# Optimization experiments

Measured on AMD Instinct MI355X. Metric: run time of the kernel, lower is better.

## Reference

```python
import jax, jax.numpy as jnp
import numpy as np

BN_EPS = 1e-5
K = 9  # 3x3 kernel positions


def conv2d(x, w, b, pad, dil=1):
    out = jax.lax.conv_general_dilated(
        x, w, window_strides=(1, 1), padding=((pad, pad), (pad, pad)),
        rhs_dilation=(dil, dil), dimension_numbers=('NCHW', 'OIHW', 'NCHW'))
    return out + b[None, :, None, None]


def bn_relu(x, g, be, mu, var):
    inv = jax.lax.rsqrt(var + BN_EPS)
    return jax.nn.relu((x - mu[None, :, None, None]) * (g * inv)[None, :, None, None] + be[None, :, None, None])


def deform_conv(x, w_om, b_om, w, b):
    # DCNv2-style modulated deformable 3x3 conv, stride 1, pad 1, dg=1.
    B, C, H, W = x.shape
    om = conv2d(x, w_om, b_om, pad=1)               # [B, 27, H, W]
    o1, o2, m = jnp.split(om, 3, axis=1)            # dy, dx, mask logits: [B,9,H,W]
    mask = jax.nn.sigmoid(m)
    ky, kx = jnp.meshgrid(jnp.arange(3), jnp.arange(3), indexing='ij')
    ky = (ky.reshape(-1) - 1).astype(x.dtype)       # kernel offsets in {-1,0,1}
    kx = (kx.reshape(-1) - 1).astype(x.dtype)
    py = jnp.arange(H, dtype=x.dtype)[None, None, :, None] + ky[None, :, None, None] + o1  # [B,9,H,W]
    px = jnp.arange(W, dtype=x.dtype)[None, None, None, :] + kx[None, :, None, None] + o2

    y0 = jnp.floor(py); x0 = jnp.floor(px)
    wy1 = py - y0; wx1 = px - x0
    y0i = y0.astype(jnp.int32); x0i = x0.astype(jnp.int32)
    x_flat = x.reshape(B, C, H * W)

    def corner(yi, xi, wgt):
        valid = ((yi >= 0) & (yi < H) & (xi >= 0) & (xi < W)).astype(x.dtype)
        idx = jnp.clip(yi, 0, H - 1) * W + jnp.clip(xi, 0, W - 1)      # [B,9,H,W]
        g = jax.vmap(lambda xf, i: xf[:, i])(x_flat, idx.reshape(B, -1))
        g = g.reshape(B, C, K, H, W)
        return g * (wgt * valid)[:, None]

    cols = (corner(y0i,     x0i,     (1 - wy1) * (1 - wx1))
            + corner(y0i,     x0i + 1, (1 - wy1) * wx1)
            + corner(y0i + 1, x0i,     wy1 * (1 - wx1))
            + corner(y0i + 1, x0i + 1, wy1 * wx1))                       # [B,C,9,H,W]
    cols = cols * mask[:, None]
    out = jnp.einsum('bckhw,ock->bohw', cols, w.reshape(w.shape[0], C, K))
    return out + b[None, :, None, None]


def setup_inputs() -> dict:
    key = jax.random.key(0)
    ks = jax.random.split(key, 24)
    B, C, H, W = 2, 64, 256, 256
    d = {}
    d['x'] = jax.random.normal(ks[0], (B, C, H, W), jnp.float32)
    d['w_om'] = jax.random.normal(ks[1], (27, C, 3, 3), jnp.float32) * 0.01
    d['b_om'] = jax.random.normal(ks[2], (27,), jnp.float32) * 0.01
    d['w_dcn'] = jax.random.normal(ks[3], (C, C, 3, 3), jnp.float32) * 0.05
    d['b_dcn'] = jax.random.normal(ks[4], (C,), jnp.float32) * 0.05
    for i, pfx in enumerate(['bn1', 'bn2', 'bn3']):
        d[pfx + '_g'] = jax.random.uniform(ks[5 + 4 * i], (C,), jnp.float32, 0.5, 1.5)
        d[pfx + '_b'] = jax.random.normal(ks[6 + 4 * i], (C,), jnp.float32) * 0.05
        d[pfx + '_m'] = jax.random.normal(ks[7 + 4 * i], (C,), jnp.float32) * 0.05
        d[pfx + '_v'] = jax.random.uniform(ks[8 + 4 * i], (C,), jnp.float32, 0.5, 1.5)
    d['w_h'] = jax.random.normal(ks[17], (C, C, 3, 3), jnp.float32) * 0.05
    d['b_h'] = jax.random.normal(ks[18], (C,), jnp.float32) * 0.05
    d['w_w'] = jax.random.normal(ks[19], (C, C, 3, 3), jnp.float32) * 0.05
    d['b_w'] = jax.random.normal(ks[20], (C,), jnp.float32) * 0.05
    d['w3'] = jax.random.normal(ks[21], (1, C, 3, 3), jnp.float32) * 0.05
    d['b3'] = jax.random.normal(ks[22], (1,), jnp.float32) * 0.05
    return d


def reference(x, w_om, b_om, w_dcn, b_dcn,
              bn1_g, bn1_b, bn1_m, bn1_v,
              w_h, b_h, bn2_g, bn2_b, bn2_m, bn2_v,
              w_w, b_w, bn3_g, bn3_b, bn3_m, bn3_v,
              w3, b3):
    h = deform_conv(x, w_om, b_om, w_dcn, b_dcn)
    h = bn_relu(h, bn1_g, bn1_b, bn1_m, bn1_v)
    h = conv2d(h, w_h, b_h, pad=2, dil=2)
    h = bn_relu(h, bn2_g, bn2_b, bn2_m, bn2_v)
    h = conv2d(h, w_w, b_w, pad=2, dil=2)
    h = bn_relu(h, bn3_g, bn3_b, bn3_m, bn3_v)
    h = conv2d(h, w3, b3, pad=1)
    return jnp.clip(jax.nn.sigmoid(h), 1e-4, 1.0 - 1e-4)
```

## Files before the change

kernel.cpp:

```cpp
#include <hip/hip_runtime.h>
#include <math.h>

#define HH 256
#define WW 256
#define HW (HH*WW)
#define NPX (2*HW)

typedef __attribute__((ext_vector_type(8))) short bf16x8;
typedef __attribute__((ext_vector_type(8))) _Float16 f16x8;
typedef __attribute__((ext_vector_type(4))) _Float16 f16x4;
typedef __attribute__((ext_vector_type(2))) _Float16 f16x2;
typedef __attribute__((ext_vector_type(4))) float f32x4;

__device__ __forceinline__ float bf2f(short h) {
    union { unsigned u; float f; } v; v.u = ((unsigned)(unsigned short)h) << 16; return v.f;
}
__device__ __forceinline__ short f2bf(float f) {
    union { float f; unsigned u; } v; v.f = f;
    unsigned r = v.u + 0x7fffu + ((v.u >> 16) & 1u);
    return (short)(r >> 16);
}
__device__ __forceinline__ short f2hs(float f) {
    _Float16 h = (_Float16)f;
    union { _Float16 h; short s; } v; v.h = h; return v.s;
}

__global__ __launch_bounds__(256) void k_x2cl(const float* __restrict__ x,
        short* __restrict__ xcl,
        const float* __restrict__ w_om, const float* __restrict__ w_dcn,
        const float* __restrict__ w_h,  const float* __restrict__ w_w,
        const float* __restrict__ w3,
        short* __restrict__ wt_om, short* __restrict__ wt_dcn,
        short* __restrict__ wt_h,  short* __restrict__ wt_w,
        float* __restrict__ w3t) {
    __shared__ short tile[256 * 70];
    const int xx = threadIdx.x;
    const int row = blockIdx.x;
    const int b = row >> 8, y = row & 255;
#pragma unroll 8
    for (int c = 0; c < 64; ++c)
        tile[xx * 70 + c] = f2hs(x[((size_t)(b * 64 + c) << 16) + (y << 8) + xx]);
    int i = blockIdx.x * 256 + threadIdx.x;
    if (i < 64 * 576) {
        int o = i / 576, k = i - o * 576, t = k >> 6, c = k & 63;
        int kb = k >> 3, j = k & 7;
        int src = (o * 64 + c) * 9 + t;
        int dst = (kb * 64 + o) * 8 + j;
        wt_dcn[dst] = f2hs(w_dcn[src]);
        wt_h[dst]   = f2bf(w_h[src]);
        wt_w[dst]   = f2bf(w_w[src]);
        if (o < 32) wt_om[(kb * 32 + o) * 8 + j] = (o < 27) ? f2hs(w_om[src]) : (short)0;
        if (o == 0) w3t[k] = w3[c * 9 + t];
    }
    __syncthreads();
    short* op = xcl + ((row << 8) + xx) * 64;
    const int* tp = (const int*)&tile[xx * 70];
#pragma unroll
    for (int j = 0; j < 8; ++j) {
        int4 v;
        v.x = tp[j * 4 + 0]; v.y = tp[j * 4 + 1];
        v.z = tp[j * 4 + 2]; v.w = tp[j * 4 + 3];
        *(int4*)(op + j * 8) = v;
    }
}

#define XPS 72

__global__ __launch_bounds__(256) __attribute__((amdgpu_waves_per_eu(2, 4)))
void k_dcn_mfma(const short* __restrict__ xcl,
        const short* __restrict__ wom, const float* __restrict__ b_om,
        const short* __restrict__ wt,
        const float* __restrict__ bias,
        const float* __restrict__ gg, const float* __restrict__ be,
        const float* __restrict__ mu, const float* __restrict__ var,
        short* __restrict__ out_cl) {
    __shared__ short xt[256 * XPS];
    __shared__ _Float16 om_lds[64 * 32];
    const int lane = threadIdx.x & 63, wave = threadIdx.x >> 6;
    const int quad = lane >> 4, l16 = lane & 15;
    const int band = blockIdx.x & 7, idx = blockIdx.x >> 3;
    const int tr = band * 8 + (idx >> 5), tc = idx & 31;
    const int b = tr >> 5;
    const int ty0 = (tr & 31) * 8, tx0 = tc * 8;
    const int base = b << 16;
    const int hy0 = ty0 - 4, hx0 = tx0 - 4;
    {
        const int p = threadIdx.x;
        const int sy = min(max(hy0 + (p >> 4), 0), 255);
        const int sx = min(max(hx0 + (p & 15), 0), 255);
        const short* src = xcl + (size_t)((base + sy * 256 + sx) * 64);
        short* dst = &xt[p * XPS];
#pragma unroll
        for (int j = 0; j < 8; ++j)
            *(bf16x8*)(dst + j * 8) = *(const bf16x8*)(src + j * 8);
    }
    __syncthreads();

    const int lp = wave * 16 + l16;
    const int pyy = lp >> 3, pxx = lp & 7;
    const int y = ty0 + pyy, x = tx0 + pxx;

    {
        f32x4 oacc[2];
        oacc[0] = (f32x4){0,0,0,0}; oacc[1] = (f32x4){0,0,0,0};
        auto loadOB = [&](int s, f16x8* Bv) {
            const int kb = s * 4 + quad;
#pragma unroll
            for (int g = 0; g < 2; ++g)
                Bv[g] = *(const f16x8*)(wom + (kb * 32 + g * 16 + l16) * 8);
        };
        f16x8 OB[2][2];
        loadOB(0, OB[0]);
#pragma unroll
        for (int s = 0; s < 18; ++s) {
            if (s < 17) loadOB(s + 1, OB[(s + 1) & 1]);
            const int t = s >> 1, c0 = (s & 1) * 32;
            const int dy = t / 3 - 1, dx = t % 3 - 1;
            f16x8 av = *(const f16x8*)&xt[((pyy + 4 + dy) * 16 + (pxx + 4 + dx)) * XPS + c0 + quad * 8];
            bool ok = ((unsigned)(y + dy) < 256u) && ((unsigned)(x + dx) < 256u);
            if (!ok) { f16x8 z = {0,0,0,0,0,0,0,0}; av = z; }
#pragma unroll
            for (int g = 0; g < 2; ++g)
                oacc[g] = __builtin_amdgcn_mfma_f32_16x16x32_f16(av, OB[s & 1][g], oacc[g], 0, 0, 0);
        }
#pragma unroll
        for (int g = 0; g < 2; ++g) {
            int o = g * 16 + l16;
            if (o < 27) {
                float bo = b_om[o];
#pragma unroll
                for (int r = 0; r < 4; ++r) {
                    float v = oacc[g][r] + bo;
                    if (o >= 18) v = 1.f / (1.f + expf(-v));
                    om_lds[(wave * 16 + quad * 4 + r) * 32 + o] = (_Float16)v;
                }
            }
        }
    }
    __syncthreads();

    f32x4 acc[4];
#pragma unroll
    for (int i = 0; i < 4; ++i) acc[i] = (f32x4){0,0,0,0};

    _Float16 omh[28];
    *(f16x8*)&omh[0]  = *(const f16x8*)&om_lds[lp * 32];
    *(f16x8*)&omh[8]  = *(const f16x8*)&om_lds[lp * 32 + 8];
    *(f16x8*)&omh[16] = *(const f16x8*)&om_lds[lp * 32 + 16];
    *(f16x4*)&omh[24] = *(const f16x4*)&om_lds[lp * 32 + 24];

    f16x8 BR0[2][4], BR1[2][4];
    auto loadBt = [&](int t, f16x8 B[2][4]) {
#pragma unroll
        for (int h = 0; h < 2; ++h) {
            const int kb = t * 8 + h * 4 + quad;
#pragma unroll
            for (int g = 0; g < 4; ++g)
                B[h][g] = *(const f16x8*)(wt + (kb * 64 + g * 16 + l16) * 8);
        }
    };
    loadBt(0, BR0);

#pragma unroll
    for (int t = 0; t < 9; ++t) {
        f16x8 (*Bc)[4] = (t & 1) ? BR1 : BR0;
        f16x8 (*Bn)[4] = (t & 1) ? BR0 : BR1;
        if (t < 8) loadBt(t + 1, Bn);

        const int ky = t / 3 - 1, kx = t % 3 - 1;
        float o1 = (float)omh[t], o2 = (float)omh[9 + t], m = (float)omh[18 + t];
        float py = (float)(y + ky) + o1;
        float px = (float)(x + kx) + o2;
        float y0f = floorf(py), x0f = floorf(px);
        float wy1 = py - y0f, wx1 = px - x0f;
        int y0 = (int)y0f, xi0 = (int)x0f, y1 = y0 + 1, xi1 = xi0 + 1;
        float w00 = (1.f - wy1) * (1.f - wx1) * m;
        float w01 = (1.f - wy1) * wx1 * m;
        float w10 = wy1 * (1.f - wx1) * m;
        float w11 = wy1 * wx1 * m;
        if (!((unsigned)y0  < 256u)) { w00 = 0.f; w01 = 0.f; }
        if (!((unsigned)y1  < 256u)) { w10 = 0.f; w11 = 0.f; }
        if (!((unsigned)xi0 < 256u)) { w00 = 0.f; w10 = 0.f; }
        if (!((unsigned)xi1 < 256u)) { w01 = 0.f; w11 = 0.f; }
        int cy0 = min(max(y0, 0), 255), cy1 = min(max(y1, 0), 255);
        int cx0 = min(max(xi0, 0), 255), cx1 = min(max(xi1, 0), 255);
        int iy0 = cy0 - hy0, iy1 = cy1 - hy0;
        int ix0 = cx0 - hx0, ix1 = cx1 - hx0;
        if (!((unsigned)iy0 < 16u)) { w00 = 0.f; w01 = 0.f; iy0 = min(max(iy0, 0), 15); }
        if (!((unsigned)iy1 < 16u)) { w10 = 0.f; w11 = 0.f; iy1 = min(max(iy1, 0), 15); }
        if (!((unsigned)ix0 < 16u)) { w00 = 0.f; w10 = 0.f; ix0 = min(max(ix0, 0), 15); }
        if (!((unsigned)ix1 < 16u)) { w01 = 0.f; w11 = 0.f; ix1 = min(max(ix1, 0), 15); }

        const int p00 = (iy0 * 16 + ix0) * XPS, p01 = (iy0 * 16 + ix1) * XPS;
        const int p10 = (iy1 * 16 + ix0) * XPS, p11 = (iy1 * 16 + ix1) * XPS;
        f16x8 C[2][4];
#pragma unroll
        for (int h = 0; h < 2; ++h) {
            const int cb = h * 32 + quad * 8;
            C[h][0] = *(const f16x8*)&xt[p00 + cb];
            C[h][1] = *(const f16x8*)&xt[p01 + cb];
            C[h][2] = *(const f16x8*)&xt[p10 + cb];
            C[h][3] = *(const f16x8*)&xt[p11 + cb];
        }
        const _Float16 h00 = (_Float16)w00, h01 = (_Float16)w01;
        const _Float16 h10 = (_Float16)w10, h11 = (_Float16)w11;
        const f16x2 W00 = {h00, h00}, W01 = {h01, h01};
        const f16x2 W10 = {h10, h10}, W11 = {h11, h11};
#pragma unroll
        for (int h = 0; h < 2; ++h) {
            const f16x2* c0 = (const f16x2*)&C[h][0];
            const f16x2* c1 = (const f16x2*)&C[h][1];
            const f16x2* c2 = (const f16x2*)&C[h][2];
            const f16x2* c3 = (const f16x2*)&C[h][3];
            f16x8 av;
            f16x2* avp = (f16x2*)&av;
#pragma unroll
            for (int d = 0; d < 4; ++d) {
                f16x2 s = c0[d] * W00;
                s = __builtin_elementwise_fma(c1[d], W01, s);
                s = __builtin_elementwise_fma(c2[d], W10, s);
                s = __builtin_elementwise_fma(c3[d], W11, s);
                avp[d] = s;
            }
#pragma unroll
            for (int g = 0; g < 4; ++g)
                acc[g] = __builtin_amdgcn_mfma_f32_16x16x32_f16(av, Bc[h][g], acc[g], 0, 0, 0);
        }
    }
#pragma unroll
    for (int g = 0; g < 4; ++g) {
        int o = g * 16 + l16;
        float sc = gg[o] * rsqrtf(var[o] + 1e-5f);
        float off = (bias[o] - mu[o]) * sc + be[o];
#pragma unroll
        for (int r = 0; r < 4; ++r) {
            int mm = quad * 4 + r;
            int pix = base + ((ty0 + wave * 2 + (mm >> 3)) << 8) + tx0 + (mm & 7);
            float v = acc[g][r] * sc + off;
            out_cl[(size_t)pix * 64 + o] = f2bf(fmaxf(v, 0.f));
        }
    }
}

__global__ __launch_bounds__(512) __attribute__((amdgpu_waves_per_eu(2, 4)))
void k_conv_mfma(const short* __restrict__ in_cl,
        const short* __restrict__ wt, const float* __restrict__ bias,
        const float* __restrict__ gg, const float* __restrict__ be,
        const float* __restrict__ mu, const float* __restrict__ var,
        short* __restrict__ out_cl) {
    __shared__ short xt[400 * XPS];
    const int lane = threadIdx.x & 63, wave = threadIdx.x >> 6;
    const int quad = lane >> 4, l16 = lane & 15;
    const int tIdx = (blockIdx.x & 7) * 64 + (blockIdx.x >> 3);
    const int tr = tIdx >> 4, tc = tIdx & 15;
    const int b = tr >> 4;
    const int ty0 = (tr & 15) * 16, tx0 = tc * 16;
    const int base = b << 16;
    for (int i = threadIdx.x; i < 400 * 8; i += 512) {
        const int p = i >> 3, j = i & 7;
        const int sy = ty0 - 2 + p / 20, sx = tx0 - 2 + p % 20;
        bf16x8 v = {0,0,0,0,0,0,0,0};
        if (((unsigned)sy < 256u) && ((unsigned)sx < 256u))
            v = *(const bf16x8*)(in_cl + (size_t)((base + sy * 256 + sx) * 64 + j * 8));
        *(bf16x8*)(&xt[p * XPS + j * 8]) = v;
    }
    __syncthreads();
    const int ly = wave * 2;
    f32x4 acc[2][4];
#pragma unroll
    for (int h = 0; h < 2; ++h)
#pragma unroll
        for (int g = 0; g < 4; ++g) acc[h][g] = (f32x4){0,0,0,0};

    auto loadB = [&](int s, bf16x8* Bv) {
        const int kb = s * 4 + quad;
#pragma unroll
        for (int g = 0; g < 4; ++g)
            Bv[g] = *(const bf16x8*)(wt + (kb * 64 + g * 16 + l16) * 8);
    };
    bf16x8 B[3][4];
    loadB(0, B[0]);
    loadB(1, B[1]);
#pragma unroll
    for (int s = 0; s < 18; ++s) {
        if (s + 2 < 18) loadB(s + 2, B[(s + 2) % 3]);
        const int t = s >> 1, c0 = (s & 1) * 32;
        const int dy = (t / 3 - 1) * 2, dx = (t % 3 - 1) * 2;
        const int cidx = c0 + quad * 8;
        bf16x8 a0 = *(const bf16x8*)&xt[((ly + 2 + dy) * 20 + (l16 + 2 + dx)) * XPS + cidx];
        bf16x8 a1 = *(const bf16x8*)&xt[((ly + 3 + dy) * 20 + (l16 + 2 + dx)) * XPS + cidx];
#pragma unroll
        for (int g = 0; g < 4; ++g) {
            acc[0][g] = __builtin_amdgcn_mfma_f32_16x16x32_bf16(a0, B[s % 3][g], acc[0][g], 0, 0, 0);
            acc[1][g] = __builtin_amdgcn_mfma_f32_16x16x32_bf16(a1, B[s % 3][g], acc[1][g], 0, 0, 0);
        }
    }
#pragma unroll
    for (int h = 0; h < 2; ++h)
#pragma unroll
    for (int g = 0; g < 4; ++g) {
        int o = g * 16 + l16;
        float sc = gg[o] * rsqrtf(var[o] + 1e-5f);
        float off = (bias[o] - mu[o]) * sc + be[o];
#pragma unroll
        for (int r = 0; r < 4; ++r) {
            int pix = base + ((ty0 + ly + h) << 8) + tx0 + quad * 4 + r;
            float v = acc[h][g][r] * sc + off;
            out_cl[(size_t)pix * 64 + o] = f2bf(fmaxf(v, 0.f));
        }
    }
}

__global__ __launch_bounds__(256) void k_final(const short* __restrict__ h_cl,
        const float* __restrict__ w3t, const float* __restrict__ b3,
        float* __restrict__ out) {
    __shared__ short xt[324 * XPS];
    const int tIdx = (blockIdx.x & 7) * 64 + (blockIdx.x >> 3);
    const int tr = tIdx >> 4, tc = tIdx & 15;
    const int b = tr >> 4;
    const int ty0 = (tr & 15) * 16, tx0 = tc * 16;
    const int base = b << 16;
    for (int i = threadIdx.x; i < 324 * 8; i += 256) {
        const int p = i >> 3, j = i & 7;
        const int sy = ty0 - 1 + p / 18, sx = tx0 - 1 + p % 18;
        bf16x8 v = {0,0,0,0,0,0,0,0};
        if (((unsigned)sy < 256u) && ((unsigned)sx < 256u))
            v = *(const bf16x8*)(h_cl + (size_t)((base + sy * 256 + sx) * 64 + j * 8));
        *(bf16x8*)(&xt[p * XPS + j * 8]) = v;
    }
    __syncthreads();
    const int ly = threadIdx.x >> 4, lx = threadIdx.x & 15;
    float a0 = 0.f, a1 = 0.f, a2 = 0.f, a3 = 0.f;
#pragma unroll
    for (int t = 0; t < 9; ++t) {
        const int hidx = (ly + 1 + t / 3 - 1) * 18 + (lx + 1 + t % 3 - 1);
        const short* hp = &xt[hidx * XPS];
        const float* wp = w3t + t * 64;
#pragma unroll
        for (int j = 0; j < 64; j += 32) {
            bf16x8 v0 = *(const bf16x8*)(hp + j);
            bf16x8 v1 = *(const bf16x8*)(hp + j + 8);
            bf16x8 v2 = *(const bf16x8*)(hp + j + 16);
            bf16x8 v3 = *(const bf16x8*)(hp + j + 24);
#pragma unroll
            for (int e = 0; e < 8; ++e) {
                a0 = fmaf(bf2f(v0[e]), wp[j + e], a0);
                a1 = fmaf(bf2f(v1[e]), wp[j + 8 + e], a1);
                a2 = fmaf(bf2f(v2[e]), wp[j + 16 + e], a2);
                a3 = fmaf(bf2f(v3[e]), wp[j + 24 + e], a3);
            }
        }
    }
    float acc = (a0 + a1) + (a2 + a3);
    float s = 1.f / (1.f + expf(-(acc + b3[0])));
    out[base + ((ty0 + ly) << 8) + tx0 + lx] = fminf(fmaxf(s, 1e-4f), 1.f - 1e-4f);
}

extern "C" void kernel_launch(void* const* d_in, const int* in_sizes, int n_in,
                              void* d_out, int out_size, void* d_ws, size_t ws_size,
                              hipStream_t stream) {
    const float* x     = (const float*)d_in[0];
    const float* w_om  = (const float*)d_in[1];
    const float* b_om  = (const float*)d_in[2];
    const float* w_dcn = (const float*)d_in[3];
    const float* b_dcn = (const float*)d_in[4];
    const float* bn1g = (const float*)d_in[5],  *bn1b = (const float*)d_in[6];
    const float* bn1m = (const float*)d_in[7],  *bn1v = (const float*)d_in[8];
    const float* bn2g = (const float*)d_in[9],  *bn2b = (const float*)d_in[10];
    const float* bn2m = (const float*)d_in[11], *bn2v = (const float*)d_in[12];
    const float* bn3g = (const float*)d_in[13], *bn3b = (const float*)d_in[14];
    const float* bn3m = (const float*)d_in[15], *bn3v = (const float*)d_in[16];
    const float* w_h = (const float*)d_in[17], *b_h = (const float*)d_in[18];
    const float* w_w = (const float*)d_in[19], *b_w = (const float*)d_in[20];
    const float* w3  = (const float*)d_in[21], *b3  = (const float*)d_in[22];
    float* outp = (float*)d_out;

    char* ws = (char*)d_ws;
    short* xcl   = (short*)ws;
    short* h1    = xcl + (size_t)NPX * 64;
    short* h2    = h1 + (size_t)NPX * 64;
    short* wt_om  = h2 + (size_t)NPX * 64;
    short* wt_dcn = wt_om  + 32 * 576;
    short* wt_h   = wt_dcn + 64 * 576;
    short* wt_w   = wt_h   + 64 * 576;
    float* w3t    = (float*)(wt_w + 64 * 576);

    dim3 blk(256);
    k_x2cl<<<512, blk, 0, stream>>>(x, xcl, w_om, w_dcn, w_h, w_w, w3,
                                    wt_om, wt_dcn, wt_h, wt_w, w3t);
    k_dcn_mfma<<<NPX / 64, blk, 0, stream>>>(xcl, wt_om, b_om, wt_dcn, b_dcn,
                                             bn1g, bn1b, bn1m, bn1v, h1);
    k_conv_mfma<<<512, dim3(512), 0, stream>>>(h1, wt_h, b_h, bn2g, bn2b, bn2m, bn2v, h2);
    k_conv_mfma<<<512, dim3(512), 0, stream>>>(h2, wt_w, b_w, bn3g, bn3b, bn3m, bn3v, h1);
    k_final<<<512, blk, 0, stream>>>(h1, w3t, b3, outp);
}
```

Before: 208.8 us.

## Shrink dilated conv tiles to 8x8 with 256-thread blocks

Changes the dilated 3x3 conv kernel from 16x16 pixel tiles handled by 512 threads to 8x8 tiles handled by 256 threads, launched as 2048 blocks. Each wave now computes one 16-pixel M block instead of two, and the LDS halo tile shrinks from 20x20 to 12x12. The aim is more blocks and higher occupancy with less LDS per block. In exchange, the halo overhead per output pixel rises (144/64 vs 400/256), and each B weight fragment is reused by only one MFMA instead of two, so weight loads per MFMA double.

After: 218.5 us. 1.05x slower.

```diff
diff --git a/kernel.cpp b/kernel.cpp
--- a/kernel.cpp
+++ b/kernel.cpp
@@ -242,35 +242,36 @@
     }
 }
 
-__global__ __launch_bounds__(512) __attribute__((amdgpu_waves_per_eu(2, 4)))
+__global__ __launch_bounds__(256)
 void k_conv_mfma(const short* __restrict__ in_cl,
         const short* __restrict__ wt, const float* __restrict__ bias,
         const float* __restrict__ gg, const float* __restrict__ be,
         const float* __restrict__ mu, const float* __restrict__ var,
         short* __restrict__ out_cl) {
-    __shared__ short xt[400 * XPS];
+    __shared__ short xt[144 * XPS];
     const int lane = threadIdx.x & 63, wave = threadIdx.x >> 6;
     const int quad = lane >> 4, l16 = lane & 15;
-    const int tIdx = (blockIdx.x & 7) * 64 + (blockIdx.x >> 3);
-    const int tr = tIdx >> 4, tc = tIdx & 15;
-    const int b = tr >> 4;
-    const int ty0 = (tr & 15) * 16, tx0 = tc * 16;
+    const int band = blockIdx.x & 7, idx = blockIdx.x >> 3;
+    const int tr = band * 8 + (idx >> 5), tc = idx & 31;
+    const int b = tr >> 5;
+    const int ty0 = (tr & 31) * 8, tx0 = tc * 8;
     const int base = b << 16;
-    for (int i = threadIdx.x; i < 400 * 8; i += 512) {
+    for (int i = threadIdx.x; i < 144 * 8; i += 256) {
         const int p = i >> 3, j = i & 7;
-        const int sy = ty0 - 2 + p / 20, sx = tx0 - 2 + p % 20;
+        const int sy = ty0 - 2 + p / 12, sx = tx0 - 2 + p % 12;
         bf16x8 v = {0,0,0,0,0,0,0,0};
         if (((unsigned)sy < 256u) && ((unsigned)sx < 256u))
             v = *(const bf16x8*)(in_cl + (size_t)((base + sy * 256 + sx) * 64 + j * 8));
         *(bf16x8*)(&xt[p * XPS + j * 8]) = v;
     }
     __syncthreads();
-    const int ly = wave * 2;
-    f32x4 acc[2][4];
-#pragma unroll
-    for (int h = 0; h < 2; ++h)
-#pragma unroll
-        for (int g = 0; g < 4; ++g) acc[h][g] = (f32x4){0,0,0,0};
+
+    const int lp = wave * 16 + l16;
+    const int pyy = lp >> 3, pxx = lp & 7;
+
+    f32x4 acc[4];
+#pragma unroll
+    for (int g = 0; g < 4; ++g) acc[g] = (f32x4){0,0,0,0};
 
     auto loadB = [&](int s, bf16x8* Bv) {
         const int kb = s * 4 + quad;
@@ -286,17 +287,11 @@
         if (s + 2 < 18) loadB(s + 2, B[(s + 2) % 3]);
         const int t = s >> 1, c0 = (s & 1) * 32;
         const int dy = (t / 3 - 1) * 2, dx = (t % 3 - 1) * 2;
-        const int cidx = c0 + quad * 8;
-        bf16x8 a0 = *(const bf16x8*)&xt[((ly + 2 + dy) * 20 + (l16 + 2 + dx)) * XPS + cidx];
-        bf16x8 a1 = *(const bf16x8*)&xt[((ly + 3 + dy) * 20 + (l16 + 2 + dx)) * XPS + cidx];
-#pragma unroll
-        for (int g = 0; g < 4; ++g) {
-            acc[0][g] = __builtin_amdgcn_mfma_f32_16x16x32_bf16(a0, B[s % 3][g], acc[0][g], 0, 0, 0);
-            acc[1][g] = __builtin_amdgcn_mfma_f32_16x16x32_bf16(a1, B[s % 3][g], acc[1][g], 0, 0, 0);
-        }
-    }
-#pragma unroll
-    for (int h = 0; h < 2; ++h)
+        bf16x8 av = *(const bf16x8*)&xt[((pyy + 2 + dy) * 12 + (pxx + 2 + dx)) * XPS + c0 + quad * 8];
+#pragma unroll
+        for (int g = 0; g < 4; ++g)
+            acc[g] = __builtin_amdgcn_mfma_f32_16x16x32_bf16(av, B[s % 3][g], acc[g], 0, 0, 0);
+    }
 #pragma unroll
     for (int g = 0; g < 4; ++g) {
         int o = g * 16 + l16;
@@ -304,8 +299,9 @@
         float off = (bias[o] - mu[o]) * sc + be[o];
 #pragma unroll
         for (int r = 0; r < 4; ++r) {
-            int pix = base + ((ty0 + ly + h) << 8) + tx0 + quad * 4 + r;
-            float v = acc[h][g][r] * sc + off;
+            int mm = quad * 4 + r;
+            int pix = base + ((ty0 + wave * 2 + (mm >> 3)) << 8) + tx0 + (mm & 7);
+            float v = acc[g][r] * sc + off;
             out_cl[(size_t)pix * 64 + o] = f2bf(fmaxf(v, 0.f));
         }
     }
@@ -390,7 +386,7 @@
                                     wt_om, wt_dcn, wt_h, wt_w, w3t);
     k_dcn_mfma<<<NPX / 64, blk, 0, stream>>>(xcl, wt_om, b_om, wt_dcn, b_dcn,
                                              bn1g, bn1b, bn1m, bn1v, h1);
-    k_conv_mfma<<<512, dim3(512), 0, stream>>>(h1, wt_h, b_h, bn2g, bn2b, bn2m, bn2v, h2);
-    k_conv_mfma<<<512, dim3(512), 0, stream>>>(h2, wt_w, b_w, bn3g, bn3b, bn3m, bn3v, h1);
+    k_conv_mfma<<<2048, blk, 0, stream>>>(h1, wt_h, b_h, bn2g, bn2b, bn2m, bn2v, h2);
+    k_conv_mfma<<<2048, blk, 0, stream>>>(h2, wt_w, b_w, bn3g, bn3b, bn3m, bn3v, h1);
     k_final<<<512, blk, 0, stream>>>(h1, w3t, b3, outp);
 }
```
